# Kernel tuning notes

Measured on AMD Instinct MI355X. Metric: run time of the kernel, lower is better.

Reference implementation:

```python
import jax, jax.numpy as jnp
import numpy as np


def _exp_levels(dx, depth):
    """Tensor-algebra exponential of a single increment dx [B, C]:
    level j is dx^{(x) j} / j!, flattened to [B, C^j]."""
    B = dx.shape[0]
    levels = [dx]
    for j in range(2, depth + 1):
        levels.append((jnp.einsum('bi,bj->bij', levels[-1], dx) / j).reshape(B, -1))
    return levels


def _chen_step(levels, dx, depth):
    """Chen's identity: sig(path * segment) = sig(path) (x) exp(dx).
    levels: tuple of [B, C^k] for k=1..depth. dx: [B, C]."""
    B = dx.shape[0]
    exps = _exp_levels(dx, depth)
    new = []
    for k in range(1, depth + 1):
        acc = levels[k - 1] + exps[k - 1]  # A_k * 1  +  1 * E_k
        for j in range(1, k):
            # A_{k-j} (x) E_j, flattened: [B, C^{k-j}] x [B, C^j] -> [B, C^k]
            acc = acc + jnp.einsum('bi,bj->bij', levels[k - j - 1], exps[j - 1]).reshape(B, -1)
        new.append(acc)
    return tuple(new)


def setup_inputs() -> dict:
    key = jax.random.key(0)
    path = jax.random.normal(key, (64, 512, 10), dtype=jnp.float32)
    return {"path": path, "depth": 4}


def reference(path, depth):
    # signature(path, depth, stream=False, basepoint=False, inverse=False,
    #           initial=None, scalar_term=False)
    dx = path[:, 1:] - path[:, :-1]  # [B, L-1, C] increments
    B = path.shape[0]
    # Initialise with the signature of the first segment: exp(dx_0).
    init = tuple(_exp_levels(dx[:, 0], depth))
    # Fold remaining segments via Chen's relation (a sequential scan; the
    # original's batch-trick is just a reassociation of this same product).
    dx_rest = jnp.swapaxes(dx[:, 1:], 0, 1)  # [L-2, B, C]

    def step(carry, d):
        return _chen_step(carry, d, depth), None

    carry, _ = jax.lax.scan(step, init, dx_rest)
    # Concatenate levels: output [B, C + C^2 + ... + C^depth]
    return jnp.concatenate(carry, axis=-1)
```

## Files before the change

kernel.cpp:

```cpp
#include <hip/hip_runtime.h>


#define CH      10
#define NSTEPS  511
#define SIGSZ   11110
#define WSSEG   11112
#define NSEG    4
#define SEGLEN  128
#define TRP     132
#define GSTEPS  32
#define NGRP    (SEGLEN / GSTEPS)

__device__ __forceinline__ float rl(float v, int lane) {
    return __int_as_float(__builtin_amdgcn_readlane(__float_as_int(v), lane));
}

__global__ __launch_bounds__(256)
void sig_partial(const float* __restrict__ path, float* __restrict__ ws) {
    __shared__ __align__(16) float flatL[SEGLEN * CH];
    __shared__ __align__(16) float trL[CH * TRP];

    const int tid  = threadIdx.x;
    const int lane = tid & 63;
    const int bx   = blockIdx.x;
    const int b    = bx >> 4;
    const int seg  = (bx >> 2) & 3;
    const int part = bx & 3;
    const int s0   = seg * SEGLEN;

    const float* p = path + (size_t)b * (512 * CH) + s0 * CH;
    for (int e = tid; e < SEGLEN * CH; e += 256) {
        const int s = e / CH;
        const int c = e - s * CH;
        float v = 0.f;
        if (s0 + s < NSTEPS) v = p[e + CH] - p[e];
        flatL[e] = v;
        trL[c * TRP + s] = v;
    }
    __syncthreads();

    const int id  = part * 256 + tid;
    const int idc = (id < 1000) ? id : 999;
    const int ci = idc / 100;
    const int cj = (idc / 10) % 10;
    const int ck = idc % 10;

    float a1 = 0.f, a2 = 0.f, a3 = 0.f;
    float a4[10];
    #pragma unroll
    for (int l = 0; l < 10; ++l) a4[l] = 0.f;

    const float* ti = trL + ci * TRP;
    const float* tj = trL + cj * TRP;
    const float* tk = trL + ck * TRP;

    for (int g = 0; g < NGRP; ++g) {
        const float* fb = flatL + g * (GSTEPS * CH);
        const float f0 = fb[lane];
        const float f1 = fb[64 + lane];
        const float f2 = fb[128 + lane];
        const float f3 = fb[192 + lane];
        const float f4 = fb[256 + lane];
        const int gs = g * GSTEPS;

        #pragma unroll
        for (int q = 0; q < GSTEPS / 4; ++q) {
            const float4 vi = *(const float4*)(ti + gs + q * 4);
            const float4 vj = *(const float4*)(tj + gs + q * 4);
            const float4 vk = *(const float4*)(tk + gs + q * 4);
            #pragma unroll
            for (int u = 0; u < 4; ++u) {
                const int sl = q * 4 + u;
                const float dxi = (u == 0) ? vi.x : (u == 1) ? vi.y
                                 : (u == 2) ? vi.z : vi.w;
                const float dxj = (u == 0) ? vj.x : (u == 1) ? vj.y
                                 : (u == 2) ? vj.z : vj.w;
                const float dxk = (u == 0) ? vk.x : (u == 1) ? vk.y
                                 : (u == 2) ? vk.z : vk.w;

                const float p1 = a1 * (1.f / 6.f) + dxi * (1.f / 24.f);
                const float q1 = a1 * 0.5f        + dxi * (1.f / 6.f);
                const float r1 = a1               + dxi * 0.5f;
                const float p2 = a2 * 0.5f + p1 * dxj;
                const float q2 = a2        + q1 * dxj;
                a2 += r1 * dxj;
                const float p3 = a3 + p2 * dxk;
                a3 += q2 * dxk;
                a1 += dxi;

                #pragma unroll
                for (int l = 0; l < 10; ++l) {
                    const int idx = sl * 10 + l;
                    const float fs = ((idx >> 6) == 0) ? f0
                                   : ((idx >> 6) == 1) ? f1
                                   : ((idx >> 6) == 2) ? f2
                                   : ((idx >> 6) == 3) ? f3 : f4;
                    a4[l] += p3 * rl(fs, idx & 63);
                }
            }
        }
    }

    if (id < 1000) {
        float* ob = ws + (size_t)(b * NSEG + seg) * WSSEG;
        float* o4 = ob + 1110 + id * 10;
        #pragma unroll
        for (int l = 0; l < 10; ++l) o4[l] = a4[l];
        ob[110 + id] = a3;
        if (ck == 0)            ob[10 + ci * 10 + cj] = a2;
        if (ck == 0 && cj == 0) ob[ci] = a1;
    }
}

__global__ __launch_bounds__(256)
void sig_combine(const float* __restrict__ ws, float* __restrict__ out) {
    __shared__ float B[1110];

    const int tid  = threadIdx.x;
    const int b    = blockIdx.x >> 2;
    const int part = blockIdx.x & 3;
    const int id   = part * 256 + tid;
    const bool valid = (id < 1000);

    const int ci = id / 100;
    const int cj = (id / 10) % 10;
    const int ck = id % 10;

    const float* w0 = ws + (size_t)b * NSEG * WSSEG;

    float a1 = 0.f, a2 = 0.f, a3 = 0.f;
    float a4[10];
    #pragma unroll
    for (int l = 0; l < 10; ++l) a4[l] = 0.f;
    if (valid) {
        a1 = w0[ci];
        a2 = w0[10 + ci * 10 + cj];
        a3 = w0[110 + id];
        #pragma unroll
        for (int l = 0; l < 10; ++l) a4[l] = w0[1110 + id * 10 + l];
    }

    for (int s = 1; s < NSEG; ++s) {
        const float* wb = w0 + (size_t)s * WSSEG;
        __syncthreads();
        for (int e = tid; e < 1110; e += 256) B[e] = wb[e];
        __syncthreads();

        if (valid) {
            const float b1i   = B[ci];
            const float b1j   = B[cj];
            const float b1k   = B[ck];
            const float b2_ij = B[10 + ci * 10 + cj];
            const float b2_jk = B[10 + cj * 10 + ck];
            const float b3ijk = B[110 + id];

            float b4v[10];
            #pragma unroll
            for (int l = 0; l < 10; ++l) b4v[l] = wb[1110 + id * 10 + l];

            #pragma unroll
            for (int l = 0; l < 10; ++l)
                a4[l] += a3 * B[l] + a2 * B[10 + ck * 10 + l]
                       + a1 * B[110 + (cj * 10 + ck) * 10 + l] + b4v[l];
            a3 += a2 * b1k + a1 * b2_jk + b3ijk;
            a2 += a1 * b1j + b2_ij;
            a1 += b1i;
        }
    }

    if (valid) {
        float* ob = out + (size_t)b * SIGSZ;
        float* o4 = ob + 1110 + id * 10;
        #pragma unroll
        for (int l = 0; l < 10; ++l) o4[l] = a4[l];
        ob[110 + id] = a3;
        if (ck == 0)            ob[10 + ci * 10 + cj] = a2;
        if (ck == 0 && cj == 0) ob[ci] = a1;
    }
}

extern "C" void kernel_launch(void* const* d_in, const int* in_sizes, int n_in,
                              void* d_out, int out_size, void* d_ws, size_t ws_size,
                              hipStream_t stream) {
    const float* path = (const float*)d_in[0];
    float* out = (float*)d_out;
    float* ws  = (float*)d_ws;

    sig_partial<<<dim3(1024), dim3(256), 0, stream>>>(path, ws);
    sig_combine<<<dim3(256),  dim3(256), 0, stream>>>(ws, out);
}
```

Baseline: 100.3 us.

## Broadcast level-4 increments via scalar loads from a padded global dx buffer

Adds a prep kernel that writes path increments into a 12-float-padded global buffer in the workspace. The partial kernel then fetches the 10 wave-uniform dx values per step with inline-asm s_load_dwordx4 into SGPRs, replacing the LDS flat copy and per-element readlane broadcasts. Lanes with id >= 1000 now skip the whole loop. In exchange it adds an extra kernel launch, and every step waits on scalar memory through s_waitcnt lgkmcnt(0), which may stall if the scalar cache misses.

```diff
diff --git a/kernel.cpp b/kernel.cpp
--- a/kernel.cpp
+++ b/kernel.cpp
@@ -8,20 +8,35 @@
 #define NSEG    4
 #define SEGLEN  128
 #define TRP     132
-#define GSTEPS  32
-#define NGRP    (SEGLEN / GSTEPS)
-
-__device__ __forceinline__ float rl(float v, int lane) {
-    return __int_as_float(__builtin_amdgcn_readlane(__float_as_int(v), lane));
-}
+
+#define DXP_OFF (64 * NSEG * WSSEG)
+
+typedef __attribute__((ext_vector_type(4))) float f32x4;
 
 __global__ __launch_bounds__(256)
-void sig_partial(const float* __restrict__ path, float* __restrict__ ws) {
-    __shared__ __align__(16) float flatL[SEGLEN * CH];
+void sig_prep(const float* __restrict__ path, float* __restrict__ dxP) {
+    const int nElem = 64 * 512 * 12;
+    for (int e = blockIdx.x * 256 + threadIdx.x; e < nElem;
+         e += gridDim.x * 256) {
+        const int row = e / 12;
+        const int c   = e - row * 12;
+        const int b   = row >> 9;
+        const int s   = row & 511;
+        float v = 0.f;
+        if (s < NSTEPS && c < CH) {
+            const float* pp = path + ((size_t)b * 512 + s) * CH + c;
+            v = pp[CH] - pp[0];
+        }
+        dxP[e] = v;
+    }
+}
+
+__global__ __launch_bounds__(256)
+void sig_partial(const float* __restrict__ path, const float* __restrict__ dxP,
+                 float* __restrict__ ws) {
     __shared__ __align__(16) float trL[CH * TRP];
 
     const int tid  = threadIdx.x;
-    const int lane = tid & 63;
     const int bx   = blockIdx.x;
     const int b    = bx >> 4;
     const int seg  = (bx >> 2) & 3;
@@ -34,43 +49,41 @@
         const int c = e - s * CH;
         float v = 0.f;
         if (s0 + s < NSTEPS) v = p[e + CH] - p[e];
-        flatL[e] = v;
         trL[c * TRP + s] = v;
     }
     __syncthreads();
 
-    const int id  = part * 256 + tid;
-    const int idc = (id < 1000) ? id : 999;
-    const int ci = idc / 100;
-    const int cj = (idc / 10) % 10;
-    const int ck = idc % 10;
-
-    float a1 = 0.f, a2 = 0.f, a3 = 0.f;
-    float a4[10];
-    #pragma unroll
-    for (int l = 0; l < 10; ++l) a4[l] = 0.f;
-
-    const float* ti = trL + ci * TRP;
-    const float* tj = trL + cj * TRP;
-    const float* tk = trL + ck * TRP;
-
-    for (int g = 0; g < NGRP; ++g) {
-        const float* fb = flatL + g * (GSTEPS * CH);
-        const float f0 = fb[lane];
-        const float f1 = fb[64 + lane];
-        const float f2 = fb[128 + lane];
-        const float f3 = fb[192 + lane];
-        const float f4 = fb[256 + lane];
-        const int gs = g * GSTEPS;
-
-        #pragma unroll
-        for (int q = 0; q < GSTEPS / 4; ++q) {
-            const float4 vi = *(const float4*)(ti + gs + q * 4);
-            const float4 vj = *(const float4*)(tj + gs + q * 4);
-            const float4 vk = *(const float4*)(tk + gs + q * 4);
+    const int id = part * 256 + tid;
+    if (id < 1000) {
+        const int ci = id / 100;
+        const int cj = (id / 10) % 10;
+        const int ck = id % 10;
+
+        float a1 = 0.f, a2 = 0.f, a3 = 0.f;
+        float a4[10];
+        #pragma unroll
+        for (int l = 0; l < 10; ++l) a4[l] = 0.f;
+
+        const float* ti = trL + ci * TRP;
+        const float* tj = trL + cj * TRP;
+        const float* tk = trL + ck * TRP;
+        const float* dp = dxP + (size_t)(b * 512 + s0) * 12;
+
+        for (int s4 = 0; s4 < SEGLEN; s4 += 4) {
+            const float4 vi = *(const float4*)(ti + s4);
+            const float4 vj = *(const float4*)(tj + s4);
+            const float4 vk = *(const float4*)(tk + s4);
             #pragma unroll
             for (int u = 0; u < 4; ++u) {
-                const int sl = q * 4 + u;
+                f32x4 eA, eB, eC;
+                asm volatile(
+                    "s_load_dwordx4 %0, %3, %4\n\t"
+                    "s_load_dwordx4 %1, %3, %5\n\t"
+                    "s_load_dwordx4 %2, %3, %6\n\t"
+                    "s_waitcnt lgkmcnt(0)"
+                    : "=s"(eA), "=s"(eB), "=s"(eC)
+                    : "s"(dp), "n"(u * 48), "n"(u * 48 + 16), "n"(u * 48 + 32));
+
                 const float dxi = (u == 0) ? vi.x : (u == 1) ? vi.y
                                  : (u == 2) ? vi.z : vi.w;
                 const float dxj = (u == 0) ? vj.x : (u == 1) ? vj.y
@@ -88,20 +101,15 @@
                 a3 += q2 * dxk;
                 a1 += dxi;
 
-                #pragma unroll
-                for (int l = 0; l < 10; ++l) {
-                    const int idx = sl * 10 + l;
-                    const float fs = ((idx >> 6) == 0) ? f0
-                                   : ((idx >> 6) == 1) ? f1
-                                   : ((idx >> 6) == 2) ? f2
-                                   : ((idx >> 6) == 3) ? f3 : f4;
-                    a4[l] += p3 * rl(fs, idx & 63);
-                }
+                a4[0] += p3 * eA.x; a4[1] += p3 * eA.y;
+                a4[2] += p3 * eA.z; a4[3] += p3 * eA.w;
+                a4[4] += p3 * eB.x; a4[5] += p3 * eB.y;
+                a4[6] += p3 * eB.z; a4[7] += p3 * eB.w;
+                a4[8] += p3 * eC.x; a4[9] += p3 * eC.y;
             }
+            dp += 48;
         }
-    }
-
-    if (id < 1000) {
+
         float* ob = ws + (size_t)(b * NSEG + seg) * WSSEG;
         float* o4 = ob + 1110 + id * 10;
         #pragma unroll
@@ -186,6 +194,10 @@
     float* out = (float*)d_out;
     float* ws  = (float*)d_ws;
 
-    sig_partial<<<dim3(1024), dim3(256), 0, stream>>>(path, ws);
-    sig_combine<<<dim3(256),  dim3(256), 0, stream>>>(ws, out);
-}
+    float* parts = ws;
+    float* dxP   = ws + DXP_OFF;
+
+    sig_prep   <<<dim3(512),  dim3(256), 0, stream>>>(path, dxP);
+    sig_partial<<<dim3(1024), dim3(256), 0, stream>>>(path, dxP, parts);
+    sig_combine<<<dim3(256),  dim3(256), 0, stream>>>(parts, out);
+}
```

Result: slower. 113.6 us (+13.3%).

## Split path into 8 segments and give each thread two k-indices sharing level-1/2 work

Applied to the files above, without the earlier changes.

The partial kernel now cuts each path into 8 segments of 64 steps instead of 4 of 128, and each thread handles a pair of k indices (ck and ck+5), so levels 1 and 2 are computed once for two level-3/4 outputs. Level-4 increments are read as float4/float2 from a padded row layout in shared memory rather than broadcast with readlane. This shortens the serial chain per block and removes redundant lower-level arithmetic. In exchange it raises register pressure with 20 level-4 accumulators and leaves a longer combine chain. The combine kernel is not shown changing with the new NSEG, so whether it handles 8 segments is unclear.

```diff
diff --git a/kernel.cpp b/kernel.cpp
--- a/kernel.cpp
+++ b/kernel.cpp
@@ -5,27 +5,20 @@
 #define NSTEPS  511
 #define SIGSZ   11110
 #define WSSEG   11112
-#define NSEG    4
-#define SEGLEN  128
-#define TRP     132
-#define GSTEPS  32
-#define NGRP    (SEGLEN / GSTEPS)
-
-__device__ __forceinline__ float rl(float v, int lane) {
-    return __int_as_float(__builtin_amdgcn_readlane(__float_as_int(v), lane));
-}
+#define NSEG    8
+#define SEGLEN  64
+#define TRP     68
 
 __global__ __launch_bounds__(256)
 void sig_partial(const float* __restrict__ path, float* __restrict__ ws) {
-    __shared__ __align__(16) float flatL[SEGLEN * CH];
+    __shared__ __align__(16) float rowL[SEGLEN * 12];
     __shared__ __align__(16) float trL[CH * TRP];
 
     const int tid  = threadIdx.x;
-    const int lane = tid & 63;
     const int bx   = blockIdx.x;
     const int b    = bx >> 4;
-    const int seg  = (bx >> 2) & 3;
-    const int part = bx & 3;
+    const int seg  = (bx >> 1) & 7;
+    const int part = bx & 1;
     const int s0   = seg * SEGLEN;
 
     const float* p = path + (size_t)b * (512 * CH) + s0 * CH;
@@ -34,79 +27,72 @@
         const int c = e - s * CH;
         float v = 0.f;
         if (s0 + s < NSTEPS) v = p[e + CH] - p[e];
-        flatL[e] = v;
+        rowL[s * 12 + c] = v;
         trL[c * TRP + s] = v;
     }
     __syncthreads();
 
-    const int id  = part * 256 + tid;
-    const int idc = (id < 1000) ? id : 999;
-    const int ci = idc / 100;
-    const int cj = (idc / 10) % 10;
-    const int ck = idc % 10;
+    const int cp = part * 256 + tid;
+    if (cp < 500) {
+        const int ci  = cp / 50;
+        const int rem = cp - ci * 50;
+        const int cj  = rem / 5;
+        const int ck  = rem - cj * 5;
 
-    float a1 = 0.f, a2 = 0.f, a3 = 0.f;
-    float a4[10];
-    #pragma unroll
-    for (int l = 0; l < 10; ++l) a4[l] = 0.f;
+        float a1 = 0.f, a2 = 0.f, a3a = 0.f, a3b = 0.f;
+        float a4a[10], a4b[10];
+        #pragma unroll
+        for (int l = 0; l < 10; ++l) { a4a[l] = 0.f; a4b[l] = 0.f; }
 
-    const float* ti = trL + ci * TRP;
-    const float* tj = trL + cj * TRP;
-    const float* tk = trL + ck * TRP;
+        const float* ti  = trL + ci * TRP;
+        const float* tj  = trL + cj * TRP;
+        const float* tk  = trL + ck * TRP;
+        const float* tk2 = trL + (ck + 5) * TRP;
 
-    for (int g = 0; g < NGRP; ++g) {
-        const float* fb = flatL + g * (GSTEPS * CH);
-        const float f0 = fb[lane];
-        const float f1 = fb[64 + lane];
-        const float f2 = fb[128 + lane];
-        const float f3 = fb[192 + lane];
-        const float f4 = fb[256 + lane];
-        const int gs = g * GSTEPS;
+        #pragma unroll 4
+        for (int s = 0; s < SEGLEN; ++s) {
+            const float* row = rowL + s * 12;
+            const float4 d0 = *(const float4*)(row);
+            const float4 d1 = *(const float4*)(row + 4);
+            const float2 d2 = *(const float2*)(row + 8);
+            const float dxi  = ti[s];
+            const float dxj  = tj[s];
+            const float dxk  = tk[s];
+            const float dxk2 = tk2[s];
 
+            const float p1 = a1 * (1.f / 6.f) + dxi * (1.f / 24.f);
+            const float q1 = a1 * 0.5f        + dxi * (1.f / 6.f);
+            const float r1 = a1               + dxi * 0.5f;
+            const float p2 = a2 * 0.5f + p1 * dxj;
+            const float q2 = a2        + q1 * dxj;
+            a2 += r1 * dxj;
+            a1 += dxi;
+
+            const float p3a = a3a + p2 * dxk;
+            a3a += q2 * dxk;
+            const float p3b = a3b + p2 * dxk2;
+            a3b += q2 * dxk2;
+
+            a4a[0] += p3a * d0.x; a4b[0] += p3b * d0.x;
+            a4a[1] += p3a * d0.y; a4b[1] += p3b * d0.y;
+            a4a[2] += p3a * d0.z; a4b[2] += p3b * d0.z;
+            a4a[3] += p3a * d0.w; a4b[3] += p3b * d0.w;
+            a4a[4] += p3a * d1.x; a4b[4] += p3b * d1.x;
+            a4a[5] += p3a * d1.y; a4b[5] += p3b * d1.y;
+            a4a[6] += p3a * d1.z; a4b[6] += p3b * d1.z;
+            a4a[7] += p3a * d1.w; a4b[7] += p3b * d1.w;
+            a4a[8] += p3a * d2.x; a4b[8] += p3b * d2.x;
+            a4a[9] += p3a * d2.y; a4b[9] += p3b * d2.y;
+        }
+
+        const int ida = ci * 100 + cj * 10 + ck;
+        float* ob = ws + (size_t)(b * NSEG + seg) * WSSEG;
+        float* o4a = ob + 1110 + ida * 10;
+        float* o4b = o4a + 50;
         #pragma unroll
-        for (int q = 0; q < GSTEPS / 4; ++q) {
-            const float4 vi = *(const float4*)(ti + gs + q * 4);
-            const float4 vj = *(const float4*)(tj + gs + q * 4);
-            const float4 vk = *(const float4*)(tk + gs + q * 4);
-            #pragma unroll
-            for (int u = 0; u < 4; ++u) {
-                const int sl = q * 4 + u;
-                const float dxi = (u == 0) ? vi.x : (u == 1) ? vi.y
-                                 : (u == 2) ? vi.z : vi.w;
-                const float dxj = (u == 0) ? vj.x : (u == 1) ? vj.y
-                                 : (u == 2) ? vj.z : vj.w;
-                const float dxk = (u == 0) ? vk.x : (u == 1) ? vk.y
-                                 : (u == 2) ? vk.z : vk.w;
-
-                const float p1 = a1 * (1.f / 6.f) + dxi * (1.f / 24.f);
-                const float q1 = a1 * 0.5f        + dxi * (1.f / 6.f);
-                const float r1 = a1               + dxi * 0.5f;
-                const float p2 = a2 * 0.5f + p1 * dxj;
-                const float q2 = a2        + q1 * dxj;
-                a2 += r1 * dxj;
-                const float p3 = a3 + p2 * dxk;
-                a3 += q2 * dxk;
-                a1 += dxi;
-
-                #pragma unroll
-                for (int l = 0; l < 10; ++l) {
-                    const int idx = sl * 10 + l;
-                    const float fs = ((idx >> 6) == 0) ? f0
-                                   : ((idx >> 6) == 1) ? f1
-                                   : ((idx >> 6) == 2) ? f2
-                                   : ((idx >> 6) == 3) ? f3 : f4;
-                    a4[l] += p3 * rl(fs, idx & 63);
-                }
-            }
-        }
-    }
-
-    if (id < 1000) {
-        float* ob = ws + (size_t)(b * NSEG + seg) * WSSEG;
-        float* o4 = ob + 1110 + id * 10;
-        #pragma unroll
-        for (int l = 0; l < 10; ++l) o4[l] = a4[l];
-        ob[110 + id] = a3;
+        for (int l = 0; l < 10; ++l) { o4a[l] = a4a[l]; o4b[l] = a4b[l]; }
+        ob[110 + ida]     = a3a;
+        ob[110 + ida + 5] = a3b;
         if (ck == 0)            ob[10 + ci * 10 + cj] = a2;
         if (ck == 0 && cj == 0) ob[ci] = a1;
     }
```

Result: faster. 97.02 us (-3.3%).
